# Kernel optimization log

Hardware: AMD Instinct MI355X
Metric: run time of the kernel (lower is better)

Reference implementation:

```python
import jax, jax.numpy as jnp
import numpy as np

N = 100_000      # nodes
E = 1_600_000    # edges (avg degree 16)
D_IN = 128
D_OUT = 128
K = 64           # low-rank attention rank


def setup_inputs() -> dict:
    key = jax.random.key(0)
    ks = jax.random.split(key, 6)
    s = lambda d: 1.0 / np.sqrt(d)
    return {
        "x": jax.random.normal(ks[0], (N, D_IN), dtype=jnp.float32),
        "edge_index": jax.random.randint(ks[1], (2, E), 0, N, dtype=jnp.int32),
        "W_gcn": jax.random.normal(ks[2], (D_IN, D_OUT), dtype=jnp.float32) * s(D_IN),
        "b_gcn": jnp.zeros((D_OUT,), jnp.float32),
        "W_att": jax.random.normal(ks[3], (D_IN, 4 * K), dtype=jnp.float32) * s(D_IN),
        "b_att": jnp.zeros((4 * K,), jnp.float32),
        "W_red": jax.random.normal(ks[4], (D_OUT + 2 * K, D_OUT), dtype=jnp.float32) * s(D_OUT + 2 * K),
        "b_red": jnp.zeros((D_OUT,), jnp.float32),
    }


def _forward(x, W_gcn, b_gcn, W_att, b_att, W_red, b_red, edge_index):
    n = x.shape[0]
    # --- GCN conv (symmetric normalization, self-loops), dropout = identity (eval) ---
    loop = jnp.arange(n, dtype=edge_index.dtype)
    src = jnp.concatenate([edge_index[0], loop])
    dst = jnp.concatenate([edge_index[1], loop])
    deg = jax.ops.segment_sum(jnp.ones_like(dst, dtype=x.dtype), dst, num_segments=n)
    dinv = jax.lax.rsqrt(deg)                      # deg >= 1 due to self-loops
    norm = dinv[src] * dinv[dst]                   # [E+n]
    h = x @ W_gcn                                  # [n, D_OUT]
    agg = jax.ops.segment_sum(h[src] * norm[:, None], dst, num_segments=n) + b_gcn
    x_local = jax.nn.relu(agg)

    # --- Low-rank global attention (LRGA) ---
    t = jax.nn.relu(x @ W_att + b_att)             # [n, 4K]
    U, V, Z, T = jnp.split(t, 4, axis=1)           # each [n, K]
    # joint_normalize2: scalar 1/mean(U @ (V^T @ 1_n))
    D = 1.0 / jnp.mean(U @ (V.T @ jnp.ones((n, 1), x.dtype)))
    res = (U @ (V.T @ Z)) * D                      # [n, K]
    x_global = jnp.concatenate([res, T], axis=1)   # [n, 2K]

    # --- fuse + dim reduce ---
    return jnp.concatenate([x_local, x_global], axis=1) @ W_red + b_red


def reference(x, edge_index, W_gcn, b_gcn, W_att, b_att, W_red, b_red):
    return _forward(x, W_gcn, b_gcn, W_att, b_att, W_red, b_red, edge_index)
```

## Files before the change

kernel.cpp:

```cpp
#include <hip/hip_runtime.h>

#define DIN   128
#define DOUT  128
#define KR    64
#define TCOLS 256
#define WCOLS 384
#define P_RED 1024
#define PSTR  4224

typedef unsigned short ushort_t;
typedef __attribute__((ext_vector_type(8))) short bf16x8;
typedef __attribute__((ext_vector_type(4))) float f32x4;

__device__ __forceinline__ float bf2f(unsigned short u) {
  return __uint_as_float(((unsigned int)u) << 16);
}
__device__ __forceinline__ unsigned short f2bf(float f) {
  unsigned int b = __float_as_uint(f);
  b = b + 0x7FFFu + ((b >> 16) & 1u);
  return (unsigned short)(b >> 16);
}

__global__ __launch_bounds__(256) void k_init(int* __restrict__ degc, float* __restrict__ VtZ,
                                              float* __restrict__ colsum, int N) {
  int i = blockIdx.x * 256 + threadIdx.x;
  if (i < N) degc[i] = 1;
  if (i < 4096) VtZ[i] = 0.f;
  if (i < 128) colsum[i] = 0.f;
}

__global__ __launch_bounds__(256) void k_deg(const int* __restrict__ ei, int* __restrict__ degc, int E) {
  int e = blockIdx.x * 256 + threadIdx.x;
  if (e < E) atomicAdd(&degc[ei[E + e]], 1);
}

__global__ __launch_bounds__(256) void k_split(const float* __restrict__ x,
                                               ushort_t* __restrict__ xh, ushort_t* __restrict__ xl4,
                                               int total4) {
  int i = blockIdx.x * 256 + threadIdx.x;
  int stride = gridDim.x * 256;
  for (; i < total4; i += stride) {
    float4 v = ((const float4*)x)[i];
    ushort4 h, l;
    h.x = f2bf(v.x); h.y = f2bf(v.y); h.z = f2bf(v.z); h.w = f2bf(v.w);
    l.x = f2bf(v.x - bf2f(h.x)); l.y = f2bf(v.y - bf2f(h.y));
    l.z = f2bf(v.z - bf2f(h.z)); l.w = f2bf(v.w - bf2f(h.w));
    ((ushort4*)xh)[i] = h;
    ((ushort4*)xl4)[i] = l;
  }
}

__global__ __launch_bounds__(128) void k_wprep(const float* __restrict__ Wg, const float* __restrict__ Wa,
                                               ushort_t* __restrict__ whT, ushort_t* __restrict__ wlT) {
  int n = blockIdx.x;
  int k = threadIdx.x;
  float v = (n < DOUT) ? Wg[(size_t)k * DOUT + n] : Wa[(size_t)k * TCOLS + (n - DOUT)];
  ushort_t h = f2bf(v);
  whT[(size_t)n * DIN + k] = h;
  wlT[(size_t)n * DIN + k] = f2bf(v - bf2f(h));
}

__global__ __launch_bounds__(256) void k_scan1(const int* __restrict__ degc, int* __restrict__ offs,
                                               int* __restrict__ bsums, int N) {
  __shared__ int s[256];
  int tid = threadIdx.x;
  int base = blockIdx.x * 1024 + tid * 4;
  int c[4], e[4];
#pragma unroll
  for (int q = 0; q < 4; ++q) c[q] = (base + q < N) ? (degc[base + q] - 1) : 0;
  e[0] = 0; e[1] = c[0]; e[2] = e[1] + c[1]; e[3] = e[2] + c[2];
  int tsum = e[3] + c[3];
  s[tid] = tsum; __syncthreads();
  for (int off = 1; off < 256; off <<= 1) {
    int v = (tid >= off) ? s[tid - off] : 0;
    __syncthreads();
    s[tid] += v;
    __syncthreads();
  }
  int tb = s[tid] - tsum;
#pragma unroll
  for (int q = 0; q < 4; ++q) if (base + q < N) offs[base + q] = tb + e[q];
  if (tid == 255) bsums[blockIdx.x] = s[255];
}

__global__ __launch_bounds__(128) void k_scan2(const int* __restrict__ bsums, int* __restrict__ boff,
                                               int* __restrict__ offs, int NBLK, int N) {
  __shared__ int s[128];
  int tid = threadIdx.x;
  int v = (tid < NBLK) ? bsums[tid] : 0;
  s[tid] = v; __syncthreads();
  for (int off = 1; off < 128; off <<= 1) {
    int u = (tid >= off) ? s[tid - off] : 0;
    __syncthreads();
    s[tid] += u;
    __syncthreads();
  }
  boff[tid] = s[tid] - v;
  if (tid == 127) offs[N] = s[127];
}

__global__ __launch_bounds__(256) void k_scan3(int* __restrict__ offs, const int* __restrict__ boff,
                                               const int* __restrict__ degc, float* __restrict__ dinv,
                                               int* __restrict__ cursor, int N) {
  int i = blockIdx.x * 256 + threadIdx.x;
  if (i < N) {
    offs[i] += boff[i >> 10];
    dinv[i] = rsqrtf((float)degc[i]);
    cursor[i] = 0;
  }
}

__global__ __launch_bounds__(256) void k_scatter(const int* __restrict__ ei, const int* __restrict__ offs,
                                                 int* __restrict__ cursor, const float* __restrict__ dinv,
                                                 int2* __restrict__ csr, int E) {
  int e = blockIdx.x * 256 + threadIdx.x;
  if (e < E) {
    int s = ei[e];
    int d = ei[E + e];
    int pos = atomicAdd(&cursor[d], 1);
    int2 q;
    q.x = s;
    q.y = __float_as_int(dinv[s] * dinv[d]);
    csr[offs[d] + pos] = q;
  }
}

__global__ __launch_bounds__(256) void k_gemm1_mfma(const ushort_t* __restrict__ xh,
                                                    const ushort_t* __restrict__ xl4,
                                                    const ushort_t* __restrict__ whT,
                                                    const ushort_t* __restrict__ wlT,
                                                    const float* __restrict__ ba,
                                                    ushort_t* __restrict__ hs, ushort_t* __restrict__ t,
                                                    int N) {
  int tid = threadIdx.x;
  int lane = tid & 63;
  int wave = tid >> 6;
  int wr = wave >> 1, wc = wave & 1;
  int colblk = blockIdx.x;
  int rowbase = blockIdx.y * 128 + wr * 64;
  int gcb = colblk * 128 + wc * 64;
  int lr = lane & 15;
  int lk = (lane >> 4) * 8;

  int rows[4];
#pragma unroll
  for (int m = 0; m < 4; ++m) {
    int r = rowbase + m * 16 + lr;
    rows[m] = (r < N) ? r : (N - 1);
  }

  f32x4 acc[4][4] = {};

#pragma unroll
  for (int s = 0; s < 4; ++s) {
    int k0 = s * 32 + lk;
    bf16x8 ah[4], al[4], bh[4], bl[4];
#pragma unroll
    for (int m = 0; m < 4; ++m) {
      ah[m] = *(const bf16x8*)&xh[(size_t)rows[m] * DIN + k0];
      al[m] = *(const bf16x8*)&xl4[(size_t)rows[m] * DIN + k0];
    }
#pragma unroll
    for (int n = 0; n < 4; ++n) {
      int gc = gcb + n * 16 + lr;
      bh[n] = *(const bf16x8*)&whT[(size_t)gc * DIN + k0];
      bl[n] = *(const bf16x8*)&wlT[(size_t)gc * DIN + k0];
    }
#pragma unroll
    for (int m = 0; m < 4; ++m)
#pragma unroll
      for (int n = 0; n < 4; ++n) {
        acc[m][n] = __builtin_amdgcn_mfma_f32_16x16x32_bf16(ah[m], bl[n], acc[m][n], 0, 0, 0);
        acc[m][n] = __builtin_amdgcn_mfma_f32_16x16x32_bf16(al[m], bh[n], acc[m][n], 0, 0, 0);
        acc[m][n] = __builtin_amdgcn_mfma_f32_16x16x32_bf16(ah[m], bh[n], acc[m][n], 0, 0, 0);
      }
  }

  int rq = (lane >> 4) * 4;
  if (colblk == 0) {
#pragma unroll
    for (int m = 0; m < 4; ++m)
#pragma unroll
      for (int i = 0; i < 4; ++i) {
        int row = rowbase + m * 16 + rq + i;
        if (row < N) {
#pragma unroll
          for (int n = 0; n < 4; ++n)
            hs[(size_t)row * DOUT + gcb + n * 16 + lr] = f2bf(acc[m][n][i]);
        }
      }
  } else {
    float bav[4];
#pragma unroll
    for (int n = 0; n < 4; ++n) bav[n] = ba[gcb - DOUT + n * 16 + lr];
#pragma unroll
    for (int m = 0; m < 4; ++m)
#pragma unroll
      for (int i = 0; i < 4; ++i) {
        int row = rowbase + m * 16 + rq + i;
        if (row < N) {
#pragma unroll
          for (int n = 0; n < 4; ++n)
            t[(size_t)row * TCOLS + gcb - DOUT + n * 16 + lr] =
                f2bf(fmaxf(acc[m][n][i] + bav[n], 0.f));
        }
      }
  }
}

__global__ __launch_bounds__(256) void k_red(const ushort_t* __restrict__ t, float* __restrict__ part,
                                             int N) {
  __shared__ float csh[512];
  int tid = threadIdx.x;
  int lane = tid & 63;
  int w = tid >> 6;
  int lr = lane & 15;
  int lk = (lane >> 4) * 8;
  int vcol = 64 + w * 16 + lr;
  int col2 = lane * 2;

  f32x4 acc[4] = {};
  float cs0 = 0.f, cs1 = 0.f;
  int ntiles = (N + 31) >> 5;

  for (int tile = blockIdx.x; tile < ntiles; tile += gridDim.x) {
    int r0 = tile * 32;
    const ushort_t* base = &t[(size_t)r0 * TCOLS];
    bf16x8 a, b[4];
    if (r0 + 32 <= N) {
#pragma unroll
      for (int j = 0; j < 8; ++j)
        ((short*)&a)[j] = (short)base[(size_t)(lk + j) * TCOLS + vcol];
#pragma unroll
      for (int n = 0; n < 4; ++n)
#pragma unroll
        for (int j = 0; j < 8; ++j)
          ((short*)&b[n])[j] = (short)base[(size_t)(lk + j) * TCOLS + 128 + n * 16 + lr];
#pragma unroll
      for (int j = 0; j < 8; ++j) {
        ushort2 u = *(const ushort2*)&base[(size_t)(w * 8 + j) * TCOLS + col2];
        cs0 += bf2f(u.x); cs1 += bf2f(u.y);
      }
    } else {
#pragma unroll
      for (int j = 0; j < 8; ++j) {
        int r = r0 + lk + j;
        ((short*)&a)[j] = (r < N) ? (short)t[(size_t)r * TCOLS + vcol] : (short)0;
      }
#pragma unroll
      for (int n = 0; n < 4; ++n)
#pragma unroll
        for (int j = 0; j < 8; ++j) {
          int r = r0 + lk + j;
          ((short*)&b[n])[j] = (r < N) ? (short)t[(size_t)r * TCOLS + 128 + n * 16 + lr] : (short)0;
        }
#pragma unroll
      for (int j = 0; j < 8; ++j) {
        int r = r0 + w * 8 + j;
        if (r < N) {
          ushort2 u = *(const ushort2*)&t[(size_t)r * TCOLS + col2];
          cs0 += bf2f(u.x); cs1 += bf2f(u.y);
        }
      }
    }
#pragma unroll
    for (int n = 0; n < 4; ++n)
      acc[n] = __builtin_amdgcn_mfma_f32_16x16x32_bf16(a, b[n], acc[n], 0, 0, 0);
  }

  float* pb = &part[(size_t)blockIdx.x * PSTR];
  int rq = (lane >> 4) * 4;
#pragma unroll
  for (int n = 0; n < 4; ++n)
#pragma unroll
    for (int i = 0; i < 4; ++i)
      pb[(w * 16 + rq + i) * 64 + n * 16 + lr] = acc[n][i];

  csh[tid] = cs0;
  csh[256 + tid] = cs1;
  __syncthreads();
  if (w == 0) {
    float t0 = csh[lane] + csh[64 + lane] + csh[128 + lane] + csh[192 + lane];
    float t1 = csh[256 + lane] + csh[320 + lane] + csh[384 + lane] + csh[448 + lane];
    pb[4096 + col2] = t0;
    pb[4096 + col2 + 1] = t1;
  }
}

__global__ __launch_bounds__(256) void k_redsum(const float* __restrict__ part,
                                                float* __restrict__ VtZ, float* __restrict__ colsum) {
  __shared__ float s[256];
  int tid = threadIdx.x;
  int j = blockIdx.x * 64 + (tid & 63);
  int bc = tid >> 6;
  float a = 0.f;
#pragma unroll 4
  for (int b = bc; b < P_RED; b += 4) a += part[(size_t)b * PSTR + j];
  s[tid] = a;
  __syncthreads();
  if (bc == 0) {
    float v = s[tid] + s[tid + 64] + s[tid + 128] + s[tid + 192];
    if (j < 4096) VtZ[j] = v;
    else colsum[j - 4096] = v;
  }
}

__global__ __launch_bounds__(64) void k_d(const float* __restrict__ colsum, float* __restrict__ Dws, int N) {
  __shared__ float s[64];
  int k = threadIdx.x;
  s[k] = colsum[k] * colsum[64 + k];
  __syncthreads();
  for (int off = 32; off > 0; off >>= 1) {
    if (k < off) s[k] += s[k + off];
    __syncthreads();
  }
  if (k == 0) {
    float p = s[0];
    Dws[0] = (p != 0.f) ? ((float)N / p) : 0.f;
  }
}

__global__ __launch_bounds__(256) void k_prep(const float* __restrict__ VtZ,
                                              const float* __restrict__ Dws,
                                              const float* __restrict__ Wr,
                                              ushort_t* __restrict__ weffT) {
  int c = blockIdx.x;
  int k = threadIdx.x;
  float v;
  if (k < 128 || k >= 192) {
    v = Wr[(size_t)k * DOUT + c];
  } else {
    float Dv = Dws[0];
    int kk = k - 128;
    float acc = 0.f;
#pragma unroll 8
    for (int j = 0; j < 64; ++j)
      acc += VtZ[kk * 64 + j] * Wr[(size_t)(128 + j) * DOUT + c];
    v = acc * Dv;
  }
  weffT[(size_t)c * 256 + k] = f2bf(v);
}

__global__ __launch_bounds__(256) void k_out_mfma(const ushort_t* __restrict__ xl,
                                                  const ushort_t* __restrict__ t,
                                                  const ushort_t* __restrict__ weffT,
                                                  const float* __restrict__ br,
                                                  float* __restrict__ out, int N) {
  int tid = threadIdx.x;
  int lane = tid & 63;
  int wave = tid >> 6;
  int wr = wave >> 1, wc = wave & 1;
  int rowbase = blockIdx.x * 128 + wr * 64;
  int cbase = wc * 64;
  int lr = lane & 15;
  int lk = (lane >> 4) * 8;

  int rows[4];
#pragma unroll
  for (int m = 0; m < 4; ++m) {
    int r = rowbase + m * 16 + lr;
    rows[m] = (r < N) ? r : (N - 1);
  }

  f32x4 acc[4][4] = {};

#pragma unroll
  for (int s = 0; s < 8; ++s) {
    int k0 = s * 32 + lk;
    bf16x8 a[4], b[4];
#pragma unroll
    for (int m = 0; m < 4; ++m) {
      const ushort_t* ap;
      if (s < 4)      ap = &xl[(size_t)rows[m] * DOUT + k0];
      else if (s < 6) ap = &t[(size_t)rows[m] * TCOLS + (k0 - 128)];
      else            ap = &t[(size_t)rows[m] * TCOLS + k0];
      a[m] = *(const bf16x8*)ap;
    }
#pragma unroll
    for (int n = 0; n < 4; ++n) {
      int c = cbase + n * 16 + lr;
      b[n] = *(const bf16x8*)&weffT[(size_t)c * 256 + k0];
    }
#pragma unroll
    for (int m = 0; m < 4; ++m)
#pragma unroll
      for (int n = 0; n < 4; ++n)
        acc[m][n] = __builtin_amdgcn_mfma_f32_16x16x32_bf16(a[m], b[n], acc[m][n], 0, 0, 0);
  }

  float brv[4];
#pragma unroll
  for (int n = 0; n < 4; ++n) brv[n] = br[cbase + n * 16 + lr];

  int rq = (lane >> 4) * 4;
#pragma unroll
  for (int m = 0; m < 4; ++m) {
#pragma unroll
    for (int i = 0; i < 4; ++i) {
      int row = rowbase + m * 16 + rq + i;
      if (row < N) {
#pragma unroll
        for (int n = 0; n < 4; ++n)
          out[(size_t)row * DOUT + cbase + n * 16 + lr] = acc[m][n][i] + brv[n];
      }
    }
  }
}

__global__ __launch_bounds__(256) void k_aggn(const ushort_t* __restrict__ hs, const int2* __restrict__ csr,
                                              const int* __restrict__ offs, const float* __restrict__ dinv,
                                              const float* __restrict__ bg,
                                              ushort_t* __restrict__ xl, int N) {
  int node = blockIdx.x * 4 + (threadIdx.x >> 6);
  int lane = threadIdx.x & 63;
  if (node >= N) return;
  int c2 = 2 * lane;
  float dn = dinv[node];
  ushort2 u = *(const ushort2*)&hs[(size_t)node * DOUT + c2];
  float a0 = dn * dn * bf2f(u.x);
  float a1 = dn * dn * bf2f(u.y);
  int e = offs[node], e1 = offs[node + 1];
  for (; e + 4 <= e1; e += 4) {
    int2 q0 = csr[e], q1 = csr[e + 1], q2 = csr[e + 2], q3 = csr[e + 3];
    ushort2 r0 = *(const ushort2*)&hs[(size_t)q0.x * DOUT + c2];
    ushort2 r1 = *(const ushort2*)&hs[(size_t)q1.x * DOUT + c2];
    ushort2 r2 = *(const ushort2*)&hs[(size_t)q2.x * DOUT + c2];
    ushort2 r3 = *(const ushort2*)&hs[(size_t)q3.x * DOUT + c2];
    float n0 = __int_as_float(q0.y), n1 = __int_as_float(q1.y);
    float n2 = __int_as_float(q2.y), n3 = __int_as_float(q3.y);
    a0 += n0 * bf2f(r0.x) + n1 * bf2f(r1.x) + n2 * bf2f(r2.x) + n3 * bf2f(r3.x);
    a1 += n0 * bf2f(r0.y) + n1 * bf2f(r1.y) + n2 * bf2f(r2.y) + n3 * bf2f(r3.y);
  }
  for (; e < e1; ++e) {
    int2 q = csr[e];
    ushort2 r = *(const ushort2*)&hs[(size_t)q.x * DOUT + c2];
    float n0 = __int_as_float(q.y);
    a0 += n0 * bf2f(r.x);
    a1 += n0 * bf2f(r.y);
  }
  ushort2 o;
  o.x = f2bf(fmaxf(a0 + bg[c2], 0.f));
  o.y = f2bf(fmaxf(a1 + bg[c2 + 1], 0.f));
  *(ushort2*)&xl[(size_t)node * DOUT + c2] = o;
}

extern "C" void kernel_launch(void* const* d_in, const int* in_sizes, int n_in,
                              void* d_out, int out_size, void* d_ws, size_t ws_size,
                              hipStream_t stream) {
  const float* x  = (const float*)d_in[0];
  const int* ei   = (const int*)d_in[1];
  const float* Wg = (const float*)d_in[2];
  const float* bg = (const float*)d_in[3];
  const float* Wa = (const float*)d_in[4];
  const float* ba = (const float*)d_in[5];
  const float* Wr = (const float*)d_in[6];
  const float* br = (const float*)d_in[7];
  float* out = (float*)d_out;

  const int N = in_sizes[0] / DIN;
  const int E = in_sizes[1] / 2;

  char* p = (char*)d_ws;
  auto alloc = [&](size_t bytes) {
    char* r = p;
    p += (bytes + 255) & ~(size_t)255;
    return r;
  };
  float* Dws    = (float*)alloc(256);
  float* colsum = (float*)alloc(128 * 4);
  float* VtZ    = (float*)alloc(4096 * 4);
  int*   bsums  = (int*)alloc(1024);
  int*   boff   = (int*)alloc(1024);
  ushort_t* weffT = (ushort_t*)alloc(128 * 256 * 2);
  ushort_t* whT = (ushort_t*)alloc((size_t)WCOLS * DIN * 2);
  ushort_t* wlT = (ushort_t*)alloc((size_t)WCOLS * DIN * 2);
  float* part   = (float*)alloc((size_t)P_RED * PSTR * 4);
  int*   degc   = (int*)alloc((size_t)N * 4);
  float* dinv   = (float*)alloc((size_t)N * 4);
  int*   offs   = (int*)alloc((size_t)(N + 1) * 4);
  int*   cursor = (int*)alloc((size_t)N * 4);
  int2*  csr    = (int2*)alloc((size_t)E * 8);
  ushort_t* xh  = (ushort_t*)alloc((size_t)N * DIN * 2);
  ushort_t* xlo = (ushort_t*)alloc((size_t)N * DIN * 2);
  ushort_t* hs  = (ushort_t*)alloc((size_t)N * DOUT * 2);
  ushort_t* t   = (ushort_t*)alloc((size_t)N * TCOLS * 2);
  ushort_t* xl  = (ushort_t*)alloc((size_t)N * DOUT * 2);
  (void)ws_size; (void)n_in; (void)out_size;

  const int GN = (N + 255) / 256;
  const int GE = (E + 255) / 256;
  const int NBLK = (N + 1023) / 1024;

  k_init<<<GN, 256, 0, stream>>>(degc, VtZ, colsum, N);
  k_deg<<<GE, 256, 0, stream>>>(ei, degc, E);
  k_split<<<2048, 256, 0, stream>>>(x, xh, xlo, N * DIN / 4);
  k_wprep<<<WCOLS, 128, 0, stream>>>(Wg, Wa, whT, wlT);
  k_scan1<<<NBLK, 256, 0, stream>>>(degc, offs, bsums, N);
  k_scan2<<<1, 128, 0, stream>>>(bsums, boff, offs, NBLK, N);
  k_scan3<<<GN, 256, 0, stream>>>(offs, boff, degc, dinv, cursor, N);
  k_scatter<<<GE, 256, 0, stream>>>(ei, offs, cursor, dinv, csr, E);
  k_gemm1_mfma<<<dim3(3, (N + 127) / 128), 256, 0, stream>>>(xh, xlo, whT, wlT, ba, hs, t, N);
  k_red<<<P_RED, 256, 0, stream>>>(t, part, N);
  k_redsum<<<PSTR / 64, 256, 0, stream>>>(part, VtZ, colsum);
  k_d<<<1, 64, 0, stream>>>(colsum, Dws, N);
  k_prep<<<128, 256, 0, stream>>>(VtZ, Dws, Wr, weffT);
  k_aggn<<<(N + 3) / 4, 256, 0, stream>>>(hs, csr, offs, dinv, bg, xl, N);
  k_out_mfma<<<(N + 127) / 128, 256, 0, stream>>>(xl, t, weffT, br, out, N);
}
```

Baseline: 517.5 us.

## Fuse bf16 hi/lo split of x into GEMM1 and make it persistent

Removes the separate k_split pass and its xh/xlo buffers; GEMM1 now reads fp32 x directly and converts it to bf16 hi/lo fragments in registers. The kernel also becomes persistent over row tiles (196 blocks per column block) with the weight fragments loaded into registers once per block. This avoids writing and re-reading two bf16 copies of x, but each of the 3 column blocks now reads and converts fp32 x, and the register-held weights raise register pressure under launch_bounds(256,2).

```diff
diff --git a/kernel.cpp b/kernel.cpp
--- a/kernel.cpp
+++ b/kernel.cpp
@@ -32,22 +32,6 @@
 __global__ __launch_bounds__(256) void k_deg(const int* __restrict__ ei, int* __restrict__ degc, int E) {
   int e = blockIdx.x * 256 + threadIdx.x;
   if (e < E) atomicAdd(&degc[ei[E + e]], 1);
-}
-
-__global__ __launch_bounds__(256) void k_split(const float* __restrict__ x,
-                                               ushort_t* __restrict__ xh, ushort_t* __restrict__ xl4,
-                                               int total4) {
-  int i = blockIdx.x * 256 + threadIdx.x;
-  int stride = gridDim.x * 256;
-  for (; i < total4; i += stride) {
-    float4 v = ((const float4*)x)[i];
-    ushort4 h, l;
-    h.x = f2bf(v.x); h.y = f2bf(v.y); h.z = f2bf(v.z); h.w = f2bf(v.w);
-    l.x = f2bf(v.x - bf2f(h.x)); l.y = f2bf(v.y - bf2f(h.y));
-    l.z = f2bf(v.z - bf2f(h.z)); l.w = f2bf(v.w - bf2f(h.w));
-    ((ushort4*)xh)[i] = h;
-    ((ushort4*)xl4)[i] = l;
-  }
 }
 
 __global__ __launch_bounds__(128) void k_wprep(const float* __restrict__ Wg, const float* __restrict__ Wa,
@@ -125,86 +109,101 @@
   }
 }
 
-__global__ __launch_bounds__(256) void k_gemm1_mfma(const ushort_t* __restrict__ xh,
-                                                    const ushort_t* __restrict__ xl4,
-                                                    const ushort_t* __restrict__ whT,
-                                                    const ushort_t* __restrict__ wlT,
-                                                    const float* __restrict__ ba,
-                                                    ushort_t* __restrict__ hs, ushort_t* __restrict__ t,
-                                                    int N) {
+__global__ __launch_bounds__(256, 2) void k_gemm1_mfma(const float* __restrict__ x,
+                                                       const ushort_t* __restrict__ whT,
+                                                       const ushort_t* __restrict__ wlT,
+                                                       const float* __restrict__ ba,
+                                                       ushort_t* __restrict__ hs, ushort_t* __restrict__ t,
+                                                       int N, int ntiles) {
   int tid = threadIdx.x;
   int lane = tid & 63;
   int wave = tid >> 6;
   int wr = wave >> 1, wc = wave & 1;
   int colblk = blockIdx.x;
-  int rowbase = blockIdx.y * 128 + wr * 64;
   int gcb = colblk * 128 + wc * 64;
   int lr = lane & 15;
   int lk = (lane >> 4) * 8;
-
-  int rows[4];
-#pragma unroll
-  for (int m = 0; m < 4; ++m) {
-    int r = rowbase + m * 16 + lr;
-    rows[m] = (r < N) ? r : (N - 1);
-  }
-
-  f32x4 acc[4][4] = {};
-
-#pragma unroll
-  for (int s = 0; s < 4; ++s) {
-    int k0 = s * 32 + lk;
-    bf16x8 ah[4], al[4], bh[4], bl[4];
-#pragma unroll
-    for (int m = 0; m < 4; ++m) {
-      ah[m] = *(const bf16x8*)&xh[(size_t)rows[m] * DIN + k0];
-      al[m] = *(const bf16x8*)&xl4[(size_t)rows[m] * DIN + k0];
-    }
+  int rq = (lane >> 4) * 4;
+
+  bf16x8 bh[4][4], bl[4][4];
+#pragma unroll
+  for (int s = 0; s < 4; ++s)
 #pragma unroll
     for (int n = 0; n < 4; ++n) {
       int gc = gcb + n * 16 + lr;
-      bh[n] = *(const bf16x8*)&whT[(size_t)gc * DIN + k0];
-      bl[n] = *(const bf16x8*)&wlT[(size_t)gc * DIN + k0];
-    }
-#pragma unroll
-    for (int m = 0; m < 4; ++m)
-#pragma unroll
-      for (int n = 0; n < 4; ++n) {
-        acc[m][n] = __builtin_amdgcn_mfma_f32_16x16x32_bf16(ah[m], bl[n], acc[m][n], 0, 0, 0);
-        acc[m][n] = __builtin_amdgcn_mfma_f32_16x16x32_bf16(al[m], bh[n], acc[m][n], 0, 0, 0);
-        acc[m][n] = __builtin_amdgcn_mfma_f32_16x16x32_bf16(ah[m], bh[n], acc[m][n], 0, 0, 0);
-      }
-  }
-
-  int rq = (lane >> 4) * 4;
-  if (colblk == 0) {
-#pragma unroll
-    for (int m = 0; m < 4; ++m)
-#pragma unroll
-      for (int i = 0; i < 4; ++i) {
-        int row = rowbase + m * 16 + rq + i;
-        if (row < N) {
-#pragma unroll
-          for (int n = 0; n < 4; ++n)
-            hs[(size_t)row * DOUT + gcb + n * 16 + lr] = f2bf(acc[m][n][i]);
+      bh[s][n] = *(const bf16x8*)&whT[(size_t)gc * DIN + s * 32 + lk];
+      bl[s][n] = *(const bf16x8*)&wlT[(size_t)gc * DIN + s * 32 + lk];
+    }
+
+  float bav[4] = {0.f, 0.f, 0.f, 0.f};
+  if (colblk > 0) {
+#pragma unroll
+    for (int n = 0; n < 4; ++n) bav[n] = ba[gcb - DOUT + n * 16 + lr];
+  }
+
+  for (int tile = blockIdx.y; tile < ntiles; tile += gridDim.y) {
+    int rowbase = tile * 128 + wr * 64;
+    int rows[4];
+#pragma unroll
+    for (int m = 0; m < 4; ++m) {
+      int r = rowbase + m * 16 + lr;
+      rows[m] = (r < N) ? r : (N - 1);
+    }
+
+    f32x4 acc[4][4] = {};
+
+#pragma unroll
+    for (int s = 0; s < 4; ++s) {
+      int k0 = s * 32 + lk;
+      bf16x8 ah[4], al[4];
+#pragma unroll
+      for (int m = 0; m < 4; ++m) {
+        float4 f0 = *(const float4*)&x[(size_t)rows[m] * DIN + k0];
+        float4 f1 = *(const float4*)&x[(size_t)rows[m] * DIN + k0 + 4];
+        float fv[8] = {f0.x, f0.y, f0.z, f0.w, f1.x, f1.y, f1.z, f1.w};
+#pragma unroll
+        for (int j = 0; j < 8; ++j) {
+          unsigned short h = f2bf(fv[j]);
+          ((short*)&ah[m])[j] = (short)h;
+          ((short*)&al[m])[j] = (short)f2bf(fv[j] - bf2f(h));
         }
       }
-  } else {
-    float bav[4];
-#pragma unroll
-    for (int n = 0; n < 4; ++n) bav[n] = ba[gcb - DOUT + n * 16 + lr];
-#pragma unroll
-    for (int m = 0; m < 4; ++m)
-#pragma unroll
-      for (int i = 0; i < 4; ++i) {
-        int row = rowbase + m * 16 + rq + i;
-        if (row < N) {
-#pragma unroll
-          for (int n = 0; n < 4; ++n)
-            t[(size_t)row * TCOLS + gcb - DOUT + n * 16 + lr] =
-                f2bf(fmaxf(acc[m][n][i] + bav[n], 0.f));
+#pragma unroll
+      for (int m = 0; m < 4; ++m)
+#pragma unroll
+        for (int n = 0; n < 4; ++n) {
+          acc[m][n] = __builtin_amdgcn_mfma_f32_16x16x32_bf16(ah[m], bl[s][n], acc[m][n], 0, 0, 0);
+          acc[m][n] = __builtin_amdgcn_mfma_f32_16x16x32_bf16(al[m], bh[s][n], acc[m][n], 0, 0, 0);
+          acc[m][n] = __builtin_amdgcn_mfma_f32_16x16x32_bf16(ah[m], bh[s][n], acc[m][n], 0, 0, 0);
         }
-      }
+    }
+
+    if (colblk == 0) {
+#pragma unroll
+      for (int m = 0; m < 4; ++m)
+#pragma unroll
+        for (int i = 0; i < 4; ++i) {
+          int row = rowbase + m * 16 + rq + i;
+          if (row < N) {
+#pragma unroll
+            for (int n = 0; n < 4; ++n)
+              hs[(size_t)row * DOUT + gcb + n * 16 + lr] = f2bf(acc[m][n][i]);
+          }
+        }
+    } else {
+#pragma unroll
+      for (int m = 0; m < 4; ++m)
+#pragma unroll
+        for (int i = 0; i < 4; ++i) {
+          int row = rowbase + m * 16 + rq + i;
+          if (row < N) {
+#pragma unroll
+            for (int n = 0; n < 4; ++n)
+              t[(size_t)row * TCOLS + gcb - DOUT + n * 16 + lr] =
+                  f2bf(fmaxf(acc[m][n][i] + bav[n], 0.f));
+          }
+        }
+    }
   }
 }
 
@@ -480,8 +479,6 @@
   int*   offs   = (int*)alloc((size_t)(N + 1) * 4);
   int*   cursor = (int*)alloc((size_t)N * 4);
   int2*  csr    = (int2*)alloc((size_t)E * 8);
-  ushort_t* xh  = (ushort_t*)alloc((size_t)N * DIN * 2);
-  ushort_t* xlo = (ushort_t*)alloc((size_t)N * DIN * 2);
   ushort_t* hs  = (ushort_t*)alloc((size_t)N * DOUT * 2);
   ushort_t* t   = (ushort_t*)alloc((size_t)N * TCOLS * 2);
   ushort_t* xl  = (ushort_t*)alloc((size_t)N * DOUT * 2);
@@ -490,16 +487,16 @@
   const int GN = (N + 255) / 256;
   const int GE = (E + 255) / 256;
   const int NBLK = (N + 1023) / 1024;
+  const int NT128 = (N + 127) / 128;
 
   k_init<<<GN, 256, 0, stream>>>(degc, VtZ, colsum, N);
   k_deg<<<GE, 256, 0, stream>>>(ei, degc, E);
-  k_split<<<2048, 256, 0, stream>>>(x, xh, xlo, N * DIN / 4);
   k_wprep<<<WCOLS, 128, 0, stream>>>(Wg, Wa, whT, wlT);
   k_scan1<<<NBLK, 256, 0, stream>>>(degc, offs, bsums, N);
   k_scan2<<<1, 128, 0, stream>>>(bsums, boff, offs, NBLK, N);
   k_scan3<<<GN, 256, 0, stream>>>(offs, boff, degc, dinv, cursor, N);
   k_scatter<<<GE, 256, 0, stream>>>(ei, offs, cursor, dinv, csr, E);
-  k_gemm1_mfma<<<dim3(3, (N + 127) / 128), 256, 0, stream>>>(xh, xlo, whT, wlT, ba, hs, t, N);
+  k_gemm1_mfma<<<dim3(3, 196), 256, 0, stream>>>(x, whT, wlT, ba, hs, t, N, NT128);
   k_red<<<P_RED, 256, 0, stream>>>(t, part, N);
   k_redsum<<<PSTR / 64, 256, 0, stream>>>(part, VtZ, colsum);
   k_d<<<1, 64, 0, stream>>>(colsum, Dws, N);
```

After: 530.4 us. 2.5% more time.
